# Kernel optimization log

Hardware: AMD Instinct MI355X
Metric: run time of the kernel (lower is better)

The kernel has to match this reference:

```python
import math
import jax, jax.numpy as jnp
import numpy as np
from jax import lax

TAU = 1.0
LAMBDA_COUNT = 1.0
ALPHA = 0.85
GAMMA = 1.0
NUM_ITER = 40


def _minpool(x, wh, ww):
    # equals -max_pool2d(-x) in torch (padding acts as +inf for min)
    return lax.reduce_window(x, jnp.inf, lax.min, (1, 1, wh, ww), (1, 1, 1, 1),
                             [(0, 0), (0, 0), (wh // 2, wh // 2), (ww // 2, ww // 2)])


def _maxpool(x, wh, ww):
    return lax.reduce_window(x, -jnp.inf, lax.max, (1, 1, wh, ww), (1, 1, 1, 1),
                             [(0, 0), (0, 0), (wh // 2, wh // 2), (ww // 2, ww // 2)])


def soft_erode(img):
    return jnp.minimum(_minpool(img, 3, 1), _minpool(img, 1, 3))


def soft_dilate(img):
    return _maxpool(img, 3, 3)


def soft_open(img):
    return soft_dilate(soft_erode(img))


def soft_skel(img):
    skel = jax.nn.relu(img - soft_open(img))

    def step(carry, _):
        img, skel = carry
        img = soft_erode(img)
        delta = jax.nn.relu(img - soft_open(img))
        skel = skel + jax.nn.relu(delta - skel * delta)
        return (img, skel), None

    (_, skel), _ = lax.scan(step, (img, skel), None, length=NUM_ITER)
    return skel


def soft_endpoints(skel):
    kernel = jnp.ones((3, 3), dtype=skel.dtype).at[1, 1].set(10.0)[None, None]  # OIHW
    neighbor_sum = lax.conv_general_dilated(skel, kernel, (1, 1), [(1, 1), (1, 1)],
                                            dimension_numbers=('NCHW', 'OIHW', 'NCHW'))
    return jnp.exp(-GAMMA * (neighbor_sum - 11.0) ** 2) * skel


def weighted_coordinates(ep):
    # ep: [B,1,H,W] -> [B,2] (y,x) weighted mean coordinates
    B, _, H, W = ep.shape
    ys = jnp.arange(H, dtype=ep.dtype)
    xs = jnp.arange(W, dtype=ep.dtype)
    total = jnp.sum(ep, axis=(1, 2, 3)) + 1e-8  # [B]
    w = ep[:, 0] / total[:, None, None]  # [B,H,W]
    yc = jnp.sum(w * ys[:, None], axis=(1, 2))
    xc = jnp.sum(w * xs[None, :], axis=(1, 2))
    return jnp.stack([yc, xc], axis=1)


def soft_dice(y_true, y_pred):
    smooth = 1.0
    inter = jnp.sum(y_true * y_pred)
    coeff = (2.0 * inter + smooth) / (jnp.sum(y_true) + jnp.sum(y_pred) + smooth)
    return 1.0 - coeff


def setup_inputs() -> dict:
    key = jax.random.key(0)
    k1, k2 = jax.random.split(key)
    network_output = jax.random.normal(k1, (8, 2, 512, 512), dtype=jnp.float32)
    y_true = jax.random.randint(k2, (8, 1, 512, 512), 0, 2).astype(jnp.int32)
    return {"network_output": network_output, "y_true": y_true}


def reference(network_output, y_true):
    B, _, H, W = network_output.shape
    pred_prob_fg = jax.nn.softmax(network_output, axis=1)[:, 1:2]  # [B,1,H,W]
    y_true_f = y_true.astype(pred_prob_fg.dtype)

    skel_pred = soft_skel(pred_prob_fg)
    skel_true = soft_skel(y_true_f)

    ep_pred = soft_endpoints(skel_pred)
    ep_true = soft_endpoints(skel_true)

    # mismatch (distance) term
    pred_coords = weighted_coordinates(ep_pred)  # [B,2]
    true_coords = weighted_coordinates(ep_true)
    dist = jnp.sqrt(jnp.sum((pred_coords - true_coords) ** 2, axis=1))
    unnormalized_distance_loss = jnp.mean(dist)

    image_diagonal = math.sqrt(H ** 2 + W ** 2)
    distance_loss = unnormalized_distance_loss / (image_diagonal * TAU + 1e-8)

    n_pred = jnp.sum(ep_pred, axis=(1, 2, 3))
    n_true = jnp.sum(ep_true, axis=(1, 2, 3))
    count_penalty = jnp.mean(jnp.abs(n_pred - n_true) / (n_pred + n_true + 1e-8))

    final_endpoint_loss = distance_loss + LAMBDA_COUNT * count_penalty
    dice = soft_dice(y_true_f, pred_prob_fg)
    return ALPHA * dice + (1.0 - ALPHA) * final_endpoint_loss
```

## Files before the change

### kernel.cpp

```cpp
#include <hip/hip_runtime.h>
#include <math.h>

#define W 512
#define H 512
#define S (W * H)
#define B 8
#define NIMG 16
#define CORE 64
#define HALO 12
#define LDT 88
#define LROWS 90
#define NQ 22
#define FINF __builtin_huge_valf()

__device__ __forceinline__ float4 ld4s(const float* p) { return *(const float4*)p; }
__device__ __forceinline__ void st4s(float* p, float4 v) { *(float4*)p = v; }

__device__ __forceinline__ float blockReduce(float v, float* sw) {
    #pragma unroll
    for (int o = 32; o; o >>= 1) v += __shfl_down(v, o, 64);
    int lane = threadIdx.x & 63, wid = threadIdx.x >> 6;
    if (lane == 0) sw[wid] = v;
    __syncthreads();
    float r = (threadIdx.x < 4) ? sw[threadIdx.x] : 0.f;
    if (wid == 0) { r += __shfl_down(r, 2, 64); r += __shfl_down(r, 1, 64); }
    __syncthreads();
    return r;
}

__global__ __launch_bounds__(256) void phase1_kernel(
        const float* __restrict__ net, const int* __restrict__ yt,
        float* __restrict__ J0, double* __restrict__ pb,
        double* __restrict__ acc) {
    __shared__ float sw[4];
    const int tid = threadIdx.x;
    if (blockIdx.x == 0 && tid < 48) acc[tid] = 0.0;
    float inter = 0.f, sp = 0.f, sy = 0.f;
    for (int i = blockIdx.x * 256 + tid; i < B * S / 4; i += 1024 * 256) {
        int b = i >> 16;
        int s = (i & 65535) << 2;
        const float* nb = net + (size_t)b * 2 * S;
        float4 x0 = ld4s(nb + s);
        float4 x1 = ld4s(nb + S + s);
        int4 yv = *(const int4*)(yt + (size_t)b * S + s);
        float4 p, yf;
        p.x = 1.f / (1.f + expf(x0.x - x1.x));
        p.y = 1.f / (1.f + expf(x0.y - x1.y));
        p.z = 1.f / (1.f + expf(x0.z - x1.z));
        p.w = 1.f / (1.f + expf(x0.w - x1.w));
        yf.x = (float)yv.x; yf.y = (float)yv.y; yf.z = (float)yv.z; yf.w = (float)yv.w;
        st4s(J0 + (size_t)b * S + s, p);
        st4s(J0 + (size_t)(B + b) * S + s, yf);
        inter += p.x * yf.x + p.y * yf.y + p.z * yf.z + p.w * yf.w;
        sp += p.x + p.y + p.z + p.w;
        sy += yf.x + yf.y + yf.z + yf.w;
    }
    float v;
    v = blockReduce(inter, sw); if (tid == 0) pb[blockIdx.x * 3 + 0] = (double)v;
    v = blockReduce(sp, sw);    if (tid == 0) pb[blockIdx.x * 3 + 1] = (double)v;
    v = blockReduce(sy, sw);    if (tid == 0) pb[blockIdx.x * 3 + 2] = (double)v;
}

template <bool INIT>
__global__ __launch_bounds__(512, 4) void skel_fused_kernel(
        const float* __restrict__ Jin, float* __restrict__ Jout,
        float* __restrict__ skel, int r0) {
    __shared__ float lds[2][LROWS * LDT];
    const int tid = threadIdx.x;
    const int lane = tid & 63;
    const int img = blockIdx.x >> 6;
    const int t64 = blockIdx.x & 63;
    const int ty = t64 >> 3, tx = t64 & 7;
    const int y0 = ty * CORE - HALO, x0 = tx * CORE - HALO;
    const float* Ji = Jin + (size_t)img * S;
    float* Jo = Jout + (size_t)img * S;
    float* Sk = skel + (size_t)img * S;
    const bool interior = (ty > 0) & (ty < 7) & (tx > 0) & (tx < 7);

    if (interior) {
        for (int i = tid; i < LDT * LDT / 4; i += 512) {
            int r = i / NQ, q = i - (i / NQ) * NQ;
            st4s(&lds[0][r * LDT + (q << 2)],
                 ld4s(Ji + (y0 + r) * W + x0 + (q << 2)));
        }
    } else {
        for (int i = tid; i < LDT * LDT / 4; i += 512) {
            int r = i / NQ, q = i - (i / NQ) * NQ;
            int gy = y0 + r, gx = x0 + (q << 2);
            float4 v;
            if ((unsigned)gy < H && (unsigned)gx < W) v = ld4s(Ji + gy * W + gx);
            else v = make_float4(FINF, FINF, FINF, FINF);
            st4s(&lds[0][r * LDT + (q << 2)], v);
        }
    }

    const int sq = tid & 15, ss = tid >> 4;
    const int tcol = HALO + (sq << 2);
    const int gxc = tx * CORE + (sq << 2);
    const int row0 = ss << 1;
    float4 sk2[2];
    #pragma unroll
    for (int j = 0; j < 2; ++j) {
        if (INIT) sk2[j] = make_float4(0.f, 0.f, 0.f, 0.f);
        else      sk2[j] = ld4s(Sk + (ty * CORE + row0 + j) * W + gxc);
    }
    __syncthreads();

    int cur = 0;
    for (int rr = r0; rr < 6; ++rr) {
        float* Jb = lds[cur];
        float* Eb = lds[cur ^ 1];
        const int rlo = 1 + 2 * rr, rhi = 86 - 2 * rr;
        const int qlo = rlo >> 2, qhi = rhi >> 2;
        const int nq = qhi - qlo + 1;
        const int nslab = (rhi - rlo + 1 + 3) >> 2;
        const int nit = nslab * nq;

        if (tid < nit) {
            int sb = tid / nq;
            int qq = qlo + (tid - sb * nq);
            int rb = rlo + (sb << 2);
            int c = qq << 2;
            const float* basep = Jb + (rb - 1) * LDT + c;
            float4 wd[6];
            #pragma unroll
            for (int j = 0; j < 6; ++j) wd[j] = ld4s(basep + j * LDT);
            float lw[4], rx[4];
            #pragma unroll
            for (int j = 0; j < 4; ++j) {
                lw[j] = __shfl_up(wd[j + 1].w, 1, 64);
                rx[j] = __shfl_down(wd[j + 1].x, 1, 64);
                if (lane == 0 && qq != qlo) lw[j] = Jb[(rb + j) * LDT + c - 1];
                if (lane == 63 && qq != qhi) rx[j] = Jb[(rb + j) * LDT + c + 4];
                if (qq == qlo) lw[j] = FINF;
                if (qq == qhi) rx[j] = FINF;
            }
            bool cOOB = false;
            int gx = x0 + c;
            if (!interior) cOOB = ((unsigned)gx >= W);
            #pragma unroll
            for (int j = 0; j < 4; ++j) {
                int r = rb + j;
                float4 a = wd[j + 1], u = wd[j], dn = wd[j + 2];
                float4 e;
                e.x = fminf(fminf(fminf(u.x, dn.x), fminf(lw[j], a.y)), a.x);
                e.y = fminf(fminf(fminf(u.y, dn.y), fminf(a.x, a.z)), a.y);
                e.z = fminf(fminf(fminf(u.z, dn.z), fminf(a.y, a.w)), a.z);
                e.w = fminf(fminf(fminf(u.w, dn.w), fminf(a.z, rx[j])), a.w);
                if (!interior) {
                    int gy = y0 + r;
                    if (((unsigned)gy >= H) | cOOB)
                        e = make_float4(FINF, FINF, FINF, FINF);
                }
                if (r <= rhi) st4s(&Eb[r * LDT + c], e);
            }
        }
        __syncthreads();

        const bool last = (rr == 5);
        {
            const float* ebase = Eb + (row0 + 11) * LDT + tcol;
            float4 E[4];
            #pragma unroll
            for (int j = 0; j < 4; ++j) E[j] = ld4s(ebase + j * LDT);
            float lwv[4], rxv[4];
            #pragma unroll
            for (int j = 0; j < 4; ++j) {
                lwv[j] = __shfl_up(E[j].w, 1, 64);
                rxv[j] = __shfl_down(E[j].x, 1, 64);
                if (sq == 0)  lwv[j] = (tx == 0) ? -FINF : Eb[(row0 + 11 + j) * LDT + 11];
                if (sq == 15) rxv[j] = (tx == 7) ? -FINF : Eb[(row0 + 11 + j) * LDT + 76];
            }
            float4 hx[4];
            #pragma unroll
            for (int j = 0; j < 4; ++j) {
                hx[j].x = fmaxf(fmaxf(lwv[j], E[j].x), E[j].y);
                hx[j].y = fmaxf(fmaxf(E[j].x, E[j].y), E[j].z);
                hx[j].z = fmaxf(fmaxf(E[j].y, E[j].z), E[j].w);
                hx[j].w = fmaxf(fmaxf(E[j].z, E[j].w), rxv[j]);
            }
            #pragma unroll
            for (int j = 0; j < 2; ++j) {
                int gy = ty * CORE + row0 + j;
                float4 hm = hx[j], hp = hx[j + 2];
                if (!interior) {
                    if (gy == 0)     hm = make_float4(-FINF, -FINF, -FINF, -FINF);
                    if (gy == H - 1) hp = make_float4(-FINF, -FINF, -FINF, -FINF);
                }
                float4 dm;
                dm.x = fmaxf(fmaxf(hm.x, hx[j + 1].x), hp.x);
                dm.y = fmaxf(fmaxf(hm.y, hx[j + 1].y), hp.y);
                dm.z = fmaxf(fmaxf(hm.z, hx[j + 1].z), hp.z);
                dm.w = fmaxf(fmaxf(hm.w, hx[j + 1].w), hp.w);
                float4 Jv = ld4s(Jb + (row0 + 12 + j) * LDT + tcol);
                float d0 = fmaxf(Jv.x - dm.x, 0.f);
                float d1 = fmaxf(Jv.y - dm.y, 0.f);
                float d2 = fmaxf(Jv.z - dm.z, 0.f);
                float d3 = fmaxf(Jv.w - dm.w, 0.f);
                sk2[j].x += fmaxf(d0 - sk2[j].x * d0, 0.f);
                sk2[j].y += fmaxf(d1 - sk2[j].y * d1, 0.f);
                sk2[j].z += fmaxf(d2 - sk2[j].z * d2, 0.f);
                sk2[j].w += fmaxf(d3 - sk2[j].w * d3, 0.f);
                if (last) {
                    st4s(Jo + gy * W + gxc, E[j + 1]);
                    st4s(Sk + gy * W + gxc, sk2[j]);
                }
            }
        }
        if (!last) __syncthreads();
        cur ^= 1;
    }
}

__global__ __launch_bounds__(256) void endpoint_kernel(
        const float* __restrict__ skel, double* __restrict__ acc) {
    __shared__ float sR[10][520];
    __shared__ float sw[4];
    const int tid = threadIdx.x;
    const int img = blockIdx.x >> 6;
    const int rb = blockIdx.x & 63;
    const int yB = rb << 3;
    const float* Sk = skel + (size_t)img * S;
    for (int i = tid; i < 1280; i += 256) {
        int r = i >> 7, c4 = i & 127;
        int gy = yB - 1 + r;
        float4 v = make_float4(0.f, 0.f, 0.f, 0.f);
        if ((unsigned)gy < H) v = ld4s(Sk + gy * W + (c4 << 2));
        st4s(&sR[r][4 + (c4 << 2)], v);
    }
    if (tid < 10) { sR[tid][3] = 0.f; sR[tid][516] = 0.f; }
    __syncthreads();
    float t = 0.f, syA = 0.f, sxA = 0.f;
    #pragma unroll
    for (int k = 0; k < 4; ++k) {
        int qidx = k * 256 + tid;
        int rrow = qidx >> 7;
        int x = (qidx & 127) << 2;
        int r = 1 + rrow;
        float gy = (float)(yB + rrow);
        const float* Rm = &sR[r - 1][4 + x];
        const float* Rc = &sR[r][4 + x];
        const float* Rp = &sR[r + 1][4 + x];
        float4 bm = ld4s(Rm); float lm = ld4s(Rm - 4).w, rm = ld4s(Rm + 4).x;
        float4 bc = ld4s(Rc); float lc = ld4s(Rc - 4).w, rc = ld4s(Rc + 4).x;
        float4 bp = ld4s(Rp); float lp = ld4s(Rp - 4).w, rp = ld4s(Rp + 4).x;
        float hm0 = lm + bm.x + bm.y, hm1 = bm.x + bm.y + bm.z;
        float hm2 = bm.y + bm.z + bm.w, hm3 = bm.z + bm.w + rm;
        float hc0 = lc + bc.x + bc.y, hc1 = bc.x + bc.y + bc.z;
        float hc2 = bc.y + bc.z + bc.w, hc3 = bc.z + bc.w + rc;
        float hp0 = lp + bp.x + bp.y, hp1 = bp.x + bp.y + bp.z;
        float hp2 = bp.y + bp.z + bp.w, hp3 = bp.z + bp.w + rp;
        float ns0 = hm0 + hc0 + hp0 + 9.f * bc.x;
        float ns1 = hm1 + hc1 + hp1 + 9.f * bc.y;
        float ns2 = hm2 + hc2 + hp2 + 9.f * bc.z;
        float ns3 = hm3 + hc3 + hp3 + 9.f * bc.w;
        float e0 = ns0 - 11.f, e1 = ns1 - 11.f, e2 = ns2 - 11.f, e3 = ns3 - 11.f;
        float ep0 = expf(-e0 * e0) * bc.x;
        float ep1 = expf(-e1 * e1) * bc.y;
        float ep2 = expf(-e2 * e2) * bc.z;
        float ep3 = expf(-e3 * e3) * bc.w;
        float es = ep0 + ep1 + ep2 + ep3;
        t += es;
        syA += gy * es;
        sxA += ep0 * (float)(x + 0) + ep1 * (float)(x + 1)
             + ep2 * (float)(x + 2) + ep3 * (float)(x + 3);
    }
    float v;
    v = blockReduce(t, sw);   if (tid == 0) atomicAdd(&acc[img * 3 + 0], (double)v);
    v = blockReduce(syA, sw); if (tid == 0) atomicAdd(&acc[img * 3 + 1], (double)v);
    v = blockReduce(sxA, sw); if (tid == 0) atomicAdd(&acc[img * 3 + 2], (double)v);
}

__global__ __launch_bounds__(256) void final_kernel(
        const double* __restrict__ acc, const double* __restrict__ pb,
        float* __restrict__ out) {
    const int tid = threadIdx.x;
    double si = 0.0, sp = 0.0, sy = 0.0;
    for (int i = tid; i < 1024; i += 256) {
        si += pb[i * 3 + 0]; sp += pb[i * 3 + 1]; sy += pb[i * 3 + 2];
    }
    #pragma unroll
    for (int o = 32; o; o >>= 1) {
        si += __shfl_down(si, o, 64);
        sp += __shfl_down(sp, o, 64);
        sy += __shfl_down(sy, o, 64);
    }
    __shared__ double dsw[3][4];
    int lane = tid & 63, wid = tid >> 6;
    if (lane == 0) { dsw[0][wid] = si; dsw[1][wid] = sp; dsw[2][wid] = sy; }
    __syncthreads();
    if (tid == 0) {
        double inter = dsw[0][0] + dsw[0][1] + dsw[0][2] + dsw[0][3];
        double sump  = dsw[1][0] + dsw[1][1] + dsw[1][2] + dsw[1][3];
        double sumy  = dsw[2][0] + dsw[2][1] + dsw[2][2] + dsw[2][3];
        double dsum = 0.0, csum = 0.0;
        for (int b = 0; b < B; ++b) {
            double tp = acc[b * 3 + 0], typ = acc[b * 3 + 1], txp = acc[b * 3 + 2];
            double tt = acc[(B + b) * 3 + 0], tyt = acc[(B + b) * 3 + 1], txt = acc[(B + b) * 3 + 2];
            double ycp = typ / (tp + 1e-8), xcp = txp / (tp + 1e-8);
            double yct = tyt / (tt + 1e-8), xct = txt / (tt + 1e-8);
            double dy = ycp - yct, dx = xcp - xct;
            dsum += sqrt(dy * dy + dx * dx);
            csum += fabs(tp - tt) / (tp + tt + 1e-8);
        }
        double diag = sqrt((double)(H * H + W * W));
        double distance_loss = (dsum / B) / (diag + 1e-8);
        double count_penalty = csum / B;
        double dice = 1.0 - (2.0 * inter + 1.0) / (sumy + sump + 1.0);
        out[0] = (float)(0.85 * dice + 0.15 * (distance_loss + count_penalty));
    }
}

extern "C" void kernel_launch(void* const* d_in, const int* in_sizes, int n_in,
                              void* d_out, int out_size, void* d_ws, size_t ws_size,
                              hipStream_t stream) {
    const float* net = (const float*)d_in[0];
    const int*   yt  = (const int*)d_in[1];
    float* out = (float*)d_out;

    float* J0   = (float*)d_ws;
    float* J1   = J0 + (size_t)NIMG * S;
    float* skel = J1 + (size_t)NIMG * S;
    double* acc = (double*)(skel + (size_t)NIMG * S);
    double* pb  = acc + 48;

    phase1_kernel<<<1024, 256, 0, stream>>>(net, yt, J0, pb, acc);

    skel_fused_kernel<true><<<NIMG * 64, 512, 0, stream>>>(J0, J1, skel, 0);
    float* a = J1; float* b = J0;
    for (int p = 1; p < 7; ++p) {
        int r0 = (p == 6) ? 1 : 0;
        skel_fused_kernel<false><<<NIMG * 64, 512, 0, stream>>>(a, b, skel, r0);
        float* tmp = a; a = b; b = tmp;
    }

    endpoint_kernel<<<NIMG * 64, 256, 0, stream>>>(skel, acc);
    final_kernel<<<1, 256, 0, stream>>>(acc, pb, out);
}
```

Before: 369.0 us.

## Use single in-place LDS buffer for skeleton stencil to raise occupancy

Replaces the double-buffered shared tile with one buffer updated in place. Each thread holds its eroded values in registers, waits at an extra barrier, then writes them back, and keeps the original J values it needs in registers. This halves LDS use per block so launch bounds can ask for 6 blocks per CU instead of 4, aiming to hide LDS latency. In exchange it adds one barrier per iteration and raises register pressure under a tighter register budget.

```diff
diff --git a/kernel.cpp b/kernel.cpp
--- a/kernel.cpp
+++ b/kernel.cpp
@@ -62,10 +62,10 @@
 }
 
 template <bool INIT>
-__global__ __launch_bounds__(512, 4) void skel_fused_kernel(
+__global__ __launch_bounds__(512, 6) void skel_fused_kernel(
         const float* __restrict__ Jin, float* __restrict__ Jout,
         float* __restrict__ skel, int r0) {
-    __shared__ float lds[2][LROWS * LDT];
+    __shared__ float Jl[LROWS * LDT];
     const int tid = threadIdx.x;
     const int lane = tid & 63;
     const int img = blockIdx.x >> 6;
@@ -80,7 +80,7 @@
     if (interior) {
         for (int i = tid; i < LDT * LDT / 4; i += 512) {
             int r = i / NQ, q = i - (i / NQ) * NQ;
-            st4s(&lds[0][r * LDT + (q << 2)],
+            st4s(&Jl[r * LDT + (q << 2)],
                  ld4s(Ji + (y0 + r) * W + x0 + (q << 2)));
         }
     } else {
@@ -90,7 +90,7 @@
             float4 v;
             if ((unsigned)gy < H && (unsigned)gx < W) v = ld4s(Ji + gy * W + gx);
             else v = make_float4(FINF, FINF, FINF, FINF);
-            st4s(&lds[0][r * LDT + (q << 2)], v);
+            st4s(&Jl[r * LDT + (q << 2)], v);
         }
     }
 
@@ -106,60 +106,63 @@
     }
     __syncthreads();
 
-    int cur = 0;
     for (int rr = r0; rr < 6; ++rr) {
-        float* Jb = lds[cur];
-        float* Eb = lds[cur ^ 1];
         const int rlo = 1 + 2 * rr, rhi = 86 - 2 * rr;
         const int qlo = rlo >> 2, qhi = rhi >> 2;
         const int nq = qhi - qlo + 1;
         const int nslab = (rhi - rlo + 1 + 3) >> 2;
         const int nit = nslab * nq;
 
-        if (tid < nit) {
+        float4 Jst0 = ld4s(Jl + (row0 + 12) * LDT + tcol);
+        float4 Jst1 = ld4s(Jl + (row0 + 13) * LDT + tcol);
+
+        float4 Ereg[4];
+        int rb = 0, cc = 0, qq = 0;
+        const bool active = (tid < nit);
+        if (active) {
             int sb = tid / nq;
-            int qq = qlo + (tid - sb * nq);
-            int rb = rlo + (sb << 2);
-            int c = qq << 2;
-            const float* basep = Jb + (rb - 1) * LDT + c;
-            float4 wd[6];
-            #pragma unroll
-            for (int j = 0; j < 6; ++j) wd[j] = ld4s(basep + j * LDT);
-            float lw[4], rx[4];
+            qq = qlo + (tid - sb * nq);
+            rb = rlo + (sb << 2);
+            cc = qq << 2;
+            const float* bp = Jl + (rb - 1) * LDT + cc;
+            float4 wA = ld4s(bp);
+            float4 wB = ld4s(bp + LDT);
+            const bool cOOB = (!interior) && ((unsigned)(x0 + cc) >= W);
             #pragma unroll
             for (int j = 0; j < 4; ++j) {
-                lw[j] = __shfl_up(wd[j + 1].w, 1, 64);
-                rx[j] = __shfl_down(wd[j + 1].x, 1, 64);
-                if (lane == 0 && qq != qlo) lw[j] = Jb[(rb + j) * LDT + c - 1];
-                if (lane == 63 && qq != qhi) rx[j] = Jb[(rb + j) * LDT + c + 4];
-                if (qq == qlo) lw[j] = FINF;
-                if (qq == qhi) rx[j] = FINF;
-            }
-            bool cOOB = false;
-            int gx = x0 + c;
-            if (!interior) cOOB = ((unsigned)gx >= W);
-            #pragma unroll
-            for (int j = 0; j < 4; ++j) {
-                int r = rb + j;
-                float4 a = wd[j + 1], u = wd[j], dn = wd[j + 2];
+                float4 wC = ld4s(bp + (j + 2) * LDT);
+                float lw = __shfl_up(wB.w, 1, 64);
+                float rx = __shfl_down(wB.x, 1, 64);
+                if (lane == 0 && qq != qlo)  lw = Jl[(rb + j) * LDT + cc - 1];
+                if (lane == 63 && qq != qhi) rx = Jl[(rb + j) * LDT + cc + 4];
+                if (qq == qlo) lw = FINF;
+                if (qq == qhi) rx = FINF;
                 float4 e;
-                e.x = fminf(fminf(fminf(u.x, dn.x), fminf(lw[j], a.y)), a.x);
-                e.y = fminf(fminf(fminf(u.y, dn.y), fminf(a.x, a.z)), a.y);
-                e.z = fminf(fminf(fminf(u.z, dn.z), fminf(a.y, a.w)), a.z);
-                e.w = fminf(fminf(fminf(u.w, dn.w), fminf(a.z, rx[j])), a.w);
+                e.x = fminf(fminf(fminf(wA.x, wC.x), fminf(lw, wB.y)), wB.x);
+                e.y = fminf(fminf(fminf(wA.y, wC.y), fminf(wB.x, wB.z)), wB.y);
+                e.z = fminf(fminf(fminf(wA.z, wC.z), fminf(wB.y, wB.w)), wB.z);
+                e.w = fminf(fminf(fminf(wA.w, wC.w), fminf(wB.z, rx)), wB.w);
                 if (!interior) {
-                    int gy = y0 + r;
+                    int gy = y0 + rb + j;
                     if (((unsigned)gy >= H) | cOOB)
                         e = make_float4(FINF, FINF, FINF, FINF);
                 }
-                if (r <= rhi) st4s(&Eb[r * LDT + c], e);
+                Ereg[j] = e;
+                wA = wB; wB = wC;
             }
+        }
+        __syncthreads();
+
+        if (active) {
+            #pragma unroll
+            for (int j = 0; j < 4; ++j)
+                if (rb + j <= rhi) st4s(&Jl[(rb + j) * LDT + cc], Ereg[j]);
         }
         __syncthreads();
 
         const bool last = (rr == 5);
         {
-            const float* ebase = Eb + (row0 + 11) * LDT + tcol;
+            const float* ebase = Jl + (row0 + 11) * LDT + tcol;
             float4 E[4];
             #pragma unroll
             for (int j = 0; j < 4; ++j) E[j] = ld4s(ebase + j * LDT);
@@ -168,8 +171,8 @@
             for (int j = 0; j < 4; ++j) {
                 lwv[j] = __shfl_up(E[j].w, 1, 64);
                 rxv[j] = __shfl_down(E[j].x, 1, 64);
-                if (sq == 0)  lwv[j] = (tx == 0) ? -FINF : Eb[(row0 + 11 + j) * LDT + 11];
-                if (sq == 15) rxv[j] = (tx == 7) ? -FINF : Eb[(row0 + 11 + j) * LDT + 76];
+                if (sq == 0)  lwv[j] = (tx == 0) ? -FINF : Jl[(row0 + 11 + j) * LDT + 11];
+                if (sq == 15) rxv[j] = (tx == 7) ? -FINF : Jl[(row0 + 11 + j) * LDT + 76];
             }
             float4 hx[4];
             #pragma unroll
@@ -192,7 +195,7 @@
                 dm.y = fmaxf(fmaxf(hm.y, hx[j + 1].y), hp.y);
                 dm.z = fmaxf(fmaxf(hm.z, hx[j + 1].z), hp.z);
                 dm.w = fmaxf(fmaxf(hm.w, hx[j + 1].w), hp.w);
-                float4 Jv = ld4s(Jb + (row0 + 12 + j) * LDT + tcol);
+                float4 Jv = (j == 0) ? Jst0 : Jst1;
                 float d0 = fmaxf(Jv.x - dm.x, 0.f);
                 float d1 = fmaxf(Jv.y - dm.y, 0.f);
                 float d2 = fmaxf(Jv.z - dm.z, 0.f);
@@ -208,7 +211,6 @@
             }
         }
         if (!last) __syncthreads();
-        cur ^= 1;
     }
 }
 
```

Result: faster. 344.7 us (-6.6%).

## Restructure skeleton kernel to compute erosion and dilation in one pass per iteration

Applied to the files above, without the earlier changes.

Reworks the fused skeleton kernel so that each pass over the LDS tile computes both the erosion of the current image and the dilation (opening) of the previous eroded image. Opening is expressed as a max over a separable 3x3 window applied directly to the eroded tile. Each thread now owns a fixed 4x4 strip across the whole tile, and only one barrier is needed per iteration instead of two. The row offset of the tile shifts by one, and the tile is computed over the full extent every pass rather than shrinking the active region. In exchange there is more redundant halo work, more edge-lane LDS reads, and more complex boundary handling.

```diff
diff --git a/kernel.cpp b/kernel.cpp
--- a/kernel.cpp
+++ b/kernel.cpp
@@ -64,151 +64,157 @@
 template <bool INIT>
 __global__ __launch_bounds__(512, 4) void skel_fused_kernel(
         const float* __restrict__ Jin, float* __restrict__ Jout,
-        float* __restrict__ skel, int r0) {
-    __shared__ float lds[2][LROWS * LDT];
+        float* __restrict__ skel, int NR) {
+    __shared__ float Jl[2][LROWS * LDT];
     const int tid = threadIdx.x;
     const int lane = tid & 63;
     const int img = blockIdx.x >> 6;
     const int t64 = blockIdx.x & 63;
     const int ty = t64 >> 3, tx = t64 & 7;
-    const int y0 = ty * CORE - HALO, x0 = tx * CORE - HALO;
+    const int yb = ty * CORE - 13;
+    const int x0 = tx * CORE - HALO;
     const float* Ji = Jin + (size_t)img * S;
     float* Jo = Jout + (size_t)img * S;
     float* Sk = skel + (size_t)img * S;
     const bool interior = (ty > 0) & (ty < 7) & (tx > 0) & (tx < 7);
 
     if (interior) {
-        for (int i = tid; i < LDT * LDT / 4; i += 512) {
+        for (int i = tid; i < LROWS * NQ; i += 512) {
             int r = i / NQ, q = i - (i / NQ) * NQ;
-            st4s(&lds[0][r * LDT + (q << 2)],
-                 ld4s(Ji + (y0 + r) * W + x0 + (q << 2)));
+            st4s(&Jl[0][r * LDT + (q << 2)],
+                 ld4s(Ji + (yb + r) * W + x0 + (q << 2)));
         }
     } else {
-        for (int i = tid; i < LDT * LDT / 4; i += 512) {
+        for (int i = tid; i < LROWS * NQ; i += 512) {
             int r = i / NQ, q = i - (i / NQ) * NQ;
-            int gy = y0 + r, gx = x0 + (q << 2);
+            int gy = yb + r, gx = x0 + (q << 2);
             float4 v;
             if ((unsigned)gy < H && (unsigned)gx < W) v = ld4s(Ji + gy * W + gx);
             else v = make_float4(FINF, FINF, FINF, FINF);
-            st4s(&lds[0][r * LDT + (q << 2)], v);
-        }
-    }
-
-    const int sq = tid & 15, ss = tid >> 4;
-    const int tcol = HALO + (sq << 2);
-    const int gxc = tx * CORE + (sq << 2);
-    const int row0 = ss << 1;
-    float4 sk2[2];
-    #pragma unroll
-    for (int j = 0; j < 2; ++j) {
-        if (INIT) sk2[j] = make_float4(0.f, 0.f, 0.f, 0.f);
-        else      sk2[j] = ld4s(Sk + (ty * CORE + row0 + j) * W + gxc);
+            st4s(&Jl[0][r * LDT + (q << 2)], v);
+        }
+    }
+
+    const int ei = tid / 22;
+    const int eq = tid - ei * 22;
+    const int erow = ei << 2;
+    const int ecol = eq << 2;
+    const int gxc = x0 + ecol;
+    const bool eact = (tid < 484);
+    const bool dilA = eact && (ei >= 3) && (ei <= 18) && (eq >= 3) && (eq <= 18);
+    const bool cOOB = (!interior) && ((unsigned)gxc >= W);
+
+    float4 sk4[4], Jc[4];
+    if (dilA) {
+        #pragma unroll
+        for (int j = 0; j < 4; ++j) {
+            if (INIT) sk4[j] = make_float4(0.f, 0.f, 0.f, 0.f);
+            else      sk4[j] = ld4s(Sk + (yb + erow + 1 + j) * W + gxc);
+        }
     }
     __syncthreads();
 
     int cur = 0;
-    for (int rr = r0; rr < 6; ++rr) {
-        float* Jb = lds[cur];
-        float* Eb = lds[cur ^ 1];
-        const int rlo = 1 + 2 * rr, rhi = 86 - 2 * rr;
-        const int qlo = rlo >> 2, qhi = rhi >> 2;
-        const int nq = qhi - qlo + 1;
-        const int nslab = (rhi - rlo + 1 + 3) >> 2;
-        const int nit = nslab * nq;
-
-        if (tid < nit) {
-            int sb = tid / nq;
-            int qq = qlo + (tid - sb * nq);
-            int rb = rlo + (sb << 2);
-            int c = qq << 2;
-            const float* basep = Jb + (rb - 1) * LDT + c;
-            float4 wd[6];
+    for (int p = 0; ; ++p) {
+        const bool doE = (p < NR);
+        const bool doD = (p > 0);
+        const float* A = Jl[cur];
+        float* Bb = Jl[cur ^ 1];
+        if (eact) {
+            const float* bp = A + erow * LDT + ecol;
+            float4 Wm = ld4s(bp);
+            float4 Wc = ld4s(bp + LDT);
             #pragma unroll
-            for (int j = 0; j < 6; ++j) wd[j] = ld4s(basep + j * LDT);
-            float lw[4], rx[4];
-            #pragma unroll
-            for (int j = 0; j < 4; ++j) {
-                lw[j] = __shfl_up(wd[j + 1].w, 1, 64);
-                rx[j] = __shfl_down(wd[j + 1].x, 1, 64);
-                if (lane == 0 && qq != qlo) lw[j] = Jb[(rb + j) * LDT + c - 1];
-                if (lane == 63 && qq != qhi) rx[j] = Jb[(rb + j) * LDT + c + 4];
-                if (qq == qlo) lw[j] = FINF;
-                if (qq == qhi) rx[j] = FINF;
+            for (int j = 1; j <= 4; ++j) {
+                float4 Wp = ld4s(bp + (j + 1) * LDT);
+                const int d = erow + j;
+                const int gy = yb + d;
+                if (doE) {
+                    float lw = __shfl_up(Wc.w, 1, 64);
+                    float rx = __shfl_down(Wc.x, 1, 64);
+                    if (lane == 0 && eq > 0)   lw = A[d * LDT + ecol - 1];
+                    if (lane == 63 && eq < 21) rx = A[d * LDT + ecol + 4];
+                    if (eq == 0)  lw = FINF;
+                    if (eq == 21) rx = FINF;
+                    float4 e;
+                    e.x = fminf(fminf(fminf(Wm.x, Wp.x), fminf(lw,   Wc.y)), Wc.x);
+                    e.y = fminf(fminf(fminf(Wm.y, Wp.y), fminf(Wc.x, Wc.z)), Wc.y);
+                    e.z = fminf(fminf(fminf(Wm.z, Wp.z), fminf(Wc.y, Wc.w)), Wc.z);
+                    e.w = fminf(fminf(fminf(Wm.w, Wp.w), fminf(Wc.z, rx  )), Wc.w);
+                    if (!interior && (((unsigned)gy >= H) | cOOB))
+                        e = make_float4(FINF, FINF, FINF, FINF);
+                    st4s(&Bb[d * LDT + ecol], e);
+                }
+                if (doD) {
+                    float4 am = Wm, ap = Wp;
+                    if (!interior) {
+                        if (gy == 0)     am = make_float4(-FINF, -FINF, -FINF, -FINF);
+                        if (gy == H - 1) ap = make_float4(-FINF, -FINF, -FINF, -FINF);
+                    }
+                    float4 vm;
+                    vm.x = fmaxf(fmaxf(am.x, ap.x), Wc.x);
+                    vm.y = fmaxf(fmaxf(am.y, ap.y), Wc.y);
+                    vm.z = fmaxf(fmaxf(am.z, ap.z), Wc.z);
+                    vm.w = fmaxf(fmaxf(am.w, ap.w), Wc.w);
+                    float lwv = __shfl_up(vm.w, 1, 64);
+                    float rxv = __shfl_down(vm.x, 1, 64);
+                    if (dilA) {
+                        if (lane == 0) {
+                            float v0 = A[(d - 1) * LDT + ecol - 1];
+                            float v1 = A[d * LDT + ecol - 1];
+                            float v2 = A[(d + 1) * LDT + ecol - 1];
+                            if (!interior) {
+                                if (gy == 0)     v0 = -FINF;
+                                if (gy == H - 1) v2 = -FINF;
+                            }
+                            lwv = fmaxf(fmaxf(v0, v1), v2);
+                        }
+                        if (lane == 63) {
+                            float v0 = A[(d - 1) * LDT + ecol + 4];
+                            float v1 = A[d * LDT + ecol + 4];
+                            float v2 = A[(d + 1) * LDT + ecol + 4];
+                            if (!interior) {
+                                if (gy == 0)     v0 = -FINF;
+                                if (gy == H - 1) v2 = -FINF;
+                            }
+                            rxv = fmaxf(fmaxf(v0, v1), v2);
+                        }
+                        if (!interior) {
+                            if (gxc == 0)     lwv = -FINF;
+                            if (gxc == W - 4) rxv = -FINF;
+                        }
+                        float4 dm;
+                        dm.x = fmaxf(fmaxf(lwv,  vm.x), vm.y);
+                        dm.y = fmaxf(fmaxf(vm.x, vm.y), vm.z);
+                        dm.z = fmaxf(fmaxf(vm.y, vm.z), vm.w);
+                        dm.w = fmaxf(fmaxf(vm.z, vm.w), rxv);
+                        float4 Jv = Jc[j - 1];
+                        float d0 = fmaxf(Jv.x - dm.x, 0.f);
+                        float d1 = fmaxf(Jv.y - dm.y, 0.f);
+                        float d2 = fmaxf(Jv.z - dm.z, 0.f);
+                        float d3 = fmaxf(Jv.w - dm.w, 0.f);
+                        sk4[j-1].x += fmaxf(d0 - sk4[j-1].x * d0, 0.f);
+                        sk4[j-1].y += fmaxf(d1 - sk4[j-1].y * d1, 0.f);
+                        sk4[j-1].z += fmaxf(d2 - sk4[j-1].z * d2, 0.f);
+                        sk4[j-1].w += fmaxf(d3 - sk4[j-1].w * d3, 0.f);
+                    }
+                }
+                Jc[j - 1] = Wc;
+                Wm = Wc; Wc = Wp;
             }
-            bool cOOB = false;
-            int gx = x0 + c;
-            if (!interior) cOOB = ((unsigned)gx >= W);
-            #pragma unroll
-            for (int j = 0; j < 4; ++j) {
-                int r = rb + j;
-                float4 a = wd[j + 1], u = wd[j], dn = wd[j + 2];
-                float4 e;
-                e.x = fminf(fminf(fminf(u.x, dn.x), fminf(lw[j], a.y)), a.x);
-                e.y = fminf(fminf(fminf(u.y, dn.y), fminf(a.x, a.z)), a.y);
-                e.z = fminf(fminf(fminf(u.z, dn.z), fminf(a.y, a.w)), a.z);
-                e.w = fminf(fminf(fminf(u.w, dn.w), fminf(a.z, rx[j])), a.w);
-                if (!interior) {
-                    int gy = y0 + r;
-                    if (((unsigned)gy >= H) | cOOB)
-                        e = make_float4(FINF, FINF, FINF, FINF);
-                }
-                if (r <= rhi) st4s(&Eb[r * LDT + c], e);
-            }
-        }
+        }
+        if (p == NR) break;
         __syncthreads();
-
-        const bool last = (rr == 5);
-        {
-            const float* ebase = Eb + (row0 + 11) * LDT + tcol;
-            float4 E[4];
-            #pragma unroll
-            for (int j = 0; j < 4; ++j) E[j] = ld4s(ebase + j * LDT);
-            float lwv[4], rxv[4];
-            #pragma unroll
-            for (int j = 0; j < 4; ++j) {
-                lwv[j] = __shfl_up(E[j].w, 1, 64);
-                rxv[j] = __shfl_down(E[j].x, 1, 64);
-                if (sq == 0)  lwv[j] = (tx == 0) ? -FINF : Eb[(row0 + 11 + j) * LDT + 11];
-                if (sq == 15) rxv[j] = (tx == 7) ? -FINF : Eb[(row0 + 11 + j) * LDT + 76];
-            }
-            float4 hx[4];
-            #pragma unroll
-            for (int j = 0; j < 4; ++j) {
-                hx[j].x = fmaxf(fmaxf(lwv[j], E[j].x), E[j].y);
-                hx[j].y = fmaxf(fmaxf(E[j].x, E[j].y), E[j].z);
-                hx[j].z = fmaxf(fmaxf(E[j].y, E[j].z), E[j].w);
-                hx[j].w = fmaxf(fmaxf(E[j].z, E[j].w), rxv[j]);
-            }
-            #pragma unroll
-            for (int j = 0; j < 2; ++j) {
-                int gy = ty * CORE + row0 + j;
-                float4 hm = hx[j], hp = hx[j + 2];
-                if (!interior) {
-                    if (gy == 0)     hm = make_float4(-FINF, -FINF, -FINF, -FINF);
-                    if (gy == H - 1) hp = make_float4(-FINF, -FINF, -FINF, -FINF);
-                }
-                float4 dm;
-                dm.x = fmaxf(fmaxf(hm.x, hx[j + 1].x), hp.x);
-                dm.y = fmaxf(fmaxf(hm.y, hx[j + 1].y), hp.y);
-                dm.z = fmaxf(fmaxf(hm.z, hx[j + 1].z), hp.z);
-                dm.w = fmaxf(fmaxf(hm.w, hx[j + 1].w), hp.w);
-                float4 Jv = ld4s(Jb + (row0 + 12 + j) * LDT + tcol);
-                float d0 = fmaxf(Jv.x - dm.x, 0.f);
-                float d1 = fmaxf(Jv.y - dm.y, 0.f);
-                float d2 = fmaxf(Jv.z - dm.z, 0.f);
-                float d3 = fmaxf(Jv.w - dm.w, 0.f);
-                sk2[j].x += fmaxf(d0 - sk2[j].x * d0, 0.f);
-                sk2[j].y += fmaxf(d1 - sk2[j].y * d1, 0.f);
-                sk2[j].z += fmaxf(d2 - sk2[j].z * d2, 0.f);
-                sk2[j].w += fmaxf(d3 - sk2[j].w * d3, 0.f);
-                if (last) {
-                    st4s(Jo + gy * W + gxc, E[j + 1]);
-                    st4s(Sk + gy * W + gxc, sk2[j]);
-                }
-            }
-        }
-        if (!last) __syncthreads();
         cur ^= 1;
+    }
+
+    if (dilA) {
+        #pragma unroll
+        for (int j = 0; j < 4; ++j) {
+            int gy = yb + erow + 1 + j;
+            st4s(Jo + gy * W + gxc, Jc[j]);
+            st4s(Sk + gy * W + gxc, sk4[j]);
+        }
     }
 }
 
@@ -326,11 +332,11 @@
 
     phase1_kernel<<<1024, 256, 0, stream>>>(net, yt, J0, pb, acc);
 
-    skel_fused_kernel<true><<<NIMG * 64, 512, 0, stream>>>(J0, J1, skel, 0);
+    skel_fused_kernel<true><<<NIMG * 64, 512, 0, stream>>>(J0, J1, skel, 6);
     float* a = J1; float* b = J0;
     for (int p = 1; p < 7; ++p) {
-        int r0 = (p == 6) ? 1 : 0;
-        skel_fused_kernel<false><<<NIMG * 64, 512, 0, stream>>>(a, b, skel, r0);
+        int nr = (p == 6) ? 5 : 6;
+        skel_fused_kernel<false><<<NIMG * 64, 512, 0, stream>>>(a, b, skel, nr);
         float* tmp = a; a = b; b = tmp;
     }
 
```

Measured after the change: 382.0 us. 3.5% more time.
